# Kernel optimization log

Hardware: AMD Instinct MI355X
Metric: run time of the kernel (lower is better)

## Reference

```python
import jax, jax.numpy as jnp
import numpy as np

HIDDEN_DIM = 1024
HEAD_DIM = 64


def setup_inputs() -> dict:
    key = jax.random.key(0)
    kx, kq, kk, kv, ko = jax.random.split(key, 5)
    B, S = 4, 4096
    x = jax.random.normal(kx, (B, S, HIDDEN_DIM), dtype=jnp.float32)
    # nn.Linear(in, out, bias=False) weight has shape [out, in]; y = x @ W.T
    scale = 1.0 / np.sqrt(HIDDEN_DIM)
    Wq = jax.random.normal(kq, (HEAD_DIM, HIDDEN_DIM), dtype=jnp.float32) * scale
    Wk = jax.random.normal(kk, (HEAD_DIM, HIDDEN_DIM), dtype=jnp.float32) * scale
    Wv = jax.random.normal(kv, (HEAD_DIM, HIDDEN_DIM), dtype=jnp.float32) * scale
    Wo = jax.random.normal(ko, (HIDDEN_DIM, HEAD_DIM), dtype=jnp.float32) * (1.0 / np.sqrt(HEAD_DIM))
    return {"x": x, "Wq": Wq, "Wk": Wk, "Wv": Wv, "Wo": Wo}


def reference(x, Wq, Wk, Wv, Wo):
    # projections: x [B,S,H] @ W.T [H,D] -> [B,S,D]
    q = jnp.einsum('bsh,dh->bsd', x, Wq)
    k = jnp.einsum('bsh,dh->bsd', x, Wk)
    v = jnp.einsum('bsh,dh->bsd', x, Wv)
    d = q.shape[-1]
    scores = jnp.einsum('bqd,bkd->bqk', q, k) / jnp.sqrt(jnp.asarray(d, q.dtype))
    S = q.shape[1]
    causal_mask = jnp.triu(jnp.ones((S, S), dtype=bool), k=1)  # True above diagonal
    scores = jnp.where(causal_mask[None, :, :], jnp.asarray(-jnp.inf, scores.dtype), scores)
    attn = jax.nn.softmax(scores, axis=-1)
    out = jnp.einsum('bqk,bkd->bqd', attn, v)
    return jnp.einsum('bsd,hd->bsh', out, Wo)
```

## Files before the change

### kernel.cpp

```cpp
#include <hip/hip_runtime.h>
#include <hip/hip_bf16.h>


typedef __attribute__((ext_vector_type(8))) __bf16 bf16x8;
typedef __attribute__((ext_vector_type(4))) float f32x4;

#define BATCH 4
#define SEQ   4096
#define HID   1024
#define HDIM  64
#define CHT   8
#define NCMAX 8

__device__ __forceinline__ unsigned short f2bf(float f) {
  unsigned u = __builtin_bit_cast(unsigned, f);
  u += 0x7fffu + ((u >> 16) & 1u);
  return (unsigned short)(u >> 16);
}
__device__ __forceinline__ float bf2f(unsigned short u) {
  unsigned v = ((unsigned)u) << 16;
  return __builtin_bit_cast(float, v);
}
__device__ __forceinline__ __bf16 f2bf16(float f) {
  unsigned short us = f2bf(f);
  return __builtin_bit_cast(__bf16, us);
}
__device__ __forceinline__ bf16x8 pack8(f32x4 a, f32x4 b) {
  bf16x8 r;
  r[0] = f2bf16(a[0]); r[1] = f2bf16(a[1]); r[2] = f2bf16(a[2]); r[3] = f2bf16(a[3]);
  r[4] = f2bf16(b[0]); r[5] = f2bf16(b[1]); r[6] = f2bf16(b[2]); r[7] = f2bf16(b[3]);
  return r;
}

__global__ __launch_bounds__(256) void convert_w(
    const float* __restrict__ Wq, const float* __restrict__ Wk,
    const float* __restrict__ Wv, const float* __restrict__ Wo,
    unsigned short* __restrict__ q, unsigned short* __restrict__ k,
    unsigned short* __restrict__ v, unsigned short* __restrict__ o) {
  const int gid = blockIdx.x * 256 + threadIdx.x;
  const int mat = gid >> 16, idx = gid & 0xFFFF;
  const float* s = (mat == 0) ? Wq : (mat == 1) ? Wk : (mat == 2) ? Wv : Wo;
  unsigned short* d = (mat == 0) ? q : (mat == 1) ? k : (mat == 2) ? v : o;
  d[idx] = f2bf(s[idx]);
}

__global__ __launch_bounds__(256) void qkv_proj(
    const float* __restrict__ x,
    const unsigned short* __restrict__ Wqb,
    const unsigned short* __restrict__ Wkb,
    const unsigned short* __restrict__ Wvb,
    unsigned short* __restrict__ Q,
    unsigned short* __restrict__ K,
    unsigned short* __restrict__ Vt) {
  const int mb   = blockIdx.x;
  const int tid  = threadIdx.x;
  const int lane = tid & 63;
  const int wave = tid >> 6;
  const int quad = lane >> 4;
  const int l15  = lane & 15;
  const int rt   = wave >> 1;
  const int nh   = wave & 1;
  const int ar   = rt * 16 + l15;
  const int row0 = mb * 32 + rt * 16;

  __shared__ float xs[2][32 * 32];

  const unsigned short* Ws[3] = {Wqb, Wkb, Wvb};

  f32x4 acc[3][2];
  const f32x4 zero = {0.f, 0.f, 0.f, 0.f};
#pragma unroll
  for (int z = 0; z < 3; ++z)
#pragma unroll
    for (int n2 = 0; n2 < 2; ++n2) acc[z][n2] = zero;

  const int srow   = tid >> 3;
  const int schunk = (tid & 7) ^ (srow & 7);
  const float* sgp = x + (size_t)(mb * 32 + srow) * HID + schunk * 4;
  float* lb0 = &xs[0][wave * 256];
  float* lb1 = &xs[1][wave * 256];

  const int ra0 = ar * 32 + ((2 * quad)     ^ (ar & 7)) * 4;
  const int ra1 = ar * 32 + ((2 * quad + 1) ^ (ar & 7)) * 4;

  __builtin_amdgcn_global_load_lds(
      (const __attribute__((address_space(1))) void*)sgp,
      (__attribute__((address_space(3))) void*)lb0, 16, 0, 0);

  for (int kk = 0; kk < HID; kk += 32) {
    const int buf = (kk >> 5) & 1;
    __syncthreads();
    if (kk + 32 < HID) {
      __builtin_amdgcn_global_load_lds(
          (const __attribute__((address_space(1))) void*)(sgp + kk + 32),
          (__attribute__((address_space(3))) void*)(buf ? lb0 : lb1), 16, 0, 0);
    }
    f32x4 alo = *reinterpret_cast<const f32x4*>(&xs[buf][ra0]);
    f32x4 ahi = *reinterpret_cast<const f32x4*>(&xs[buf][ra1]);
    bf16x8 a = pack8(alo, ahi);
#pragma unroll
    for (int z = 0; z < 3; ++z)
#pragma unroll
      for (int n2 = 0; n2 < 2; ++n2) {
        const int col = nh * 32 + n2 * 16 + l15;
        bf16x8 b = *reinterpret_cast<const bf16x8*>(Ws[z] + (size_t)col * HID + kk + quad * 8);
        acc[z][n2] = __builtin_amdgcn_mfma_f32_16x16x32_bf16(a, b, acc[z][n2], 0, 0, 0);
      }
  }

#pragma unroll
  for (int z = 0; z < 2; ++z) {
    unsigned short* Out = (z == 0) ? Q : K;
#pragma unroll
    for (int n2 = 0; n2 < 2; ++n2)
#pragma unroll
      for (int r = 0; r < 4; ++r) {
        const int row = row0 + quad * 4 + r;
        const int col = nh * 32 + n2 * 16 + l15;
        Out[(size_t)row * HDIM + col] = f2bf(acc[z][n2][r]);
      }
  }
#pragma unroll
  for (int n2 = 0; n2 < 2; ++n2)
#pragma unroll
    for (int r = 0; r < 4; ++r) {
      const int row = row0 + quad * 4 + r;
      const int col = nh * 32 + n2 * 16 + l15;
      const int bb = row >> 12, sl = row & 4095;
      Vt[(size_t)bb * HDIM * SEQ + (size_t)col * SEQ + sl] = f2bf(acc[2][n2][r]);
    }
}

#define LSTR 72

__global__ __launch_bounds__(256) void flash_splitk(
    const unsigned short* __restrict__ Qg,
    const unsigned short* __restrict__ Kg,
    const unsigned short* __restrict__ Vt,
    unsigned short* __restrict__ Og,
    unsigned short* __restrict__ Opart,
    float2* __restrict__ Ml) {
  const int qb = blockIdx.x;
  const int b  = blockIdx.y;
  const int c  = blockIdx.z;
  const int nc = (qb >> 3) + 1;
  if (c >= nc) return;
  const int j0 = c * CHT;
  const int j1 = min(j0 + CHT, qb + 1);

  const int tid  = threadIdx.x;
  const int lane = tid & 63;
  const int wave = tid >> 6;
  const int quad = lane >> 4;
  const int l15  = lane & 15;

  __shared__ unsigned short kt[64 * LSTR];
  __shared__ unsigned short vt[64 * LSTR];
  __shared__ unsigned short pt[4][16 * LSTR];

  const size_t base  = (size_t)b * SEQ * HDIM;
  const size_t baseT = (size_t)b * HDIM * SEQ;
  const int qrow0 = qb * 64 + wave * 16;

  bf16x8 aq[2];
  {
    const unsigned short* qp = Qg + base + (size_t)(qrow0 + l15) * HDIM + quad * 8;
    aq[0] = *reinterpret_cast<const bf16x8*>(qp);
    aq[1] = *reinterpret_cast<const bf16x8*>(qp + 32);
  }

  f32x4 o[4];
  const f32x4 zero = {0.f, 0.f, 0.f, 0.f};
#pragma unroll
  for (int n = 0; n < 4; ++n) o[n] = zero;
  float m_i[4], l_i[4];
#pragma unroll
  for (int r = 0; r < 4; ++r) { m_i[r] = -__builtin_inff(); l_i[r] = 0.f; }

  unsigned short* pw = pt[wave];
  const int srow = tid >> 2, sc0 = (tid & 3) * 16;
  const unsigned short* kb = Kg + base;
  const unsigned short* vb = Vt + baseT;

  const float C = 0.125f * 1.44269504f;

  uint4 pk0, pk1, pv0, pv1;
  {
    const uint4* kp = reinterpret_cast<const uint4*>(kb + (size_t)(j0 * 64 + srow) * HDIM + sc0);
    pk0 = kp[0]; pk1 = kp[1];
    const uint4* vp = reinterpret_cast<const uint4*>(vb + (size_t)srow * SEQ + j0 * 64 + sc0);
    pv0 = vp[0]; pv1 = vp[1];
    *reinterpret_cast<uint4*>(&kt[srow * LSTR + sc0])     = pk0;
    *reinterpret_cast<uint4*>(&kt[srow * LSTR + sc0 + 8]) = pk1;
    *reinterpret_cast<uint4*>(&vt[srow * LSTR + sc0])     = pv0;
    *reinterpret_cast<uint4*>(&vt[srow * LSTR + sc0 + 8]) = pv1;
  }

  for (int j = j0; j < j1; ++j) {
    __syncthreads();
    const bool pre = (j + 1 < j1);
    if (pre) {
      const uint4* kp = reinterpret_cast<const uint4*>(kb + (size_t)((j + 1) * 64 + srow) * HDIM + sc0);
      pk0 = kp[0]; pk1 = kp[1];
      const uint4* vp = reinterpret_cast<const uint4*>(vb + (size_t)srow * SEQ + (j + 1) * 64 + sc0);
      pv0 = vp[0]; pv1 = vp[1];
    }

    f32x4 s[4];
#pragma unroll
    for (int n = 0; n < 4; ++n) s[n] = zero;
#pragma unroll
    for (int ks = 0; ks < 2; ++ks) {
#pragma unroll
      for (int n = 0; n < 4; ++n) {
        bf16x8 bk = *reinterpret_cast<const bf16x8*>(&kt[(n * 16 + l15) * LSTR + ks * 32 + quad * 8]);
        s[n] = __builtin_amdgcn_mfma_f32_16x16x32_bf16(aq[ks], bk, s[n], 0, 0, 0);
      }
    }

    if (j == qb) {
#pragma unroll
      for (int n = 0; n < 4; ++n) {
        const int col = n * 16 + l15;
#pragma unroll
        for (int r = 0; r < 4; ++r) {
          const int rowl = wave * 16 + quad * 4 + r;
          if (col > rowl) s[n][r] = -__builtin_inff();
        }
      }
    }

    float mnew[4], alpha[4], mC[4];
#pragma unroll
    for (int r = 0; r < 4; ++r) {
      float v = fmaxf(fmaxf(s[0][r], s[1][r]), fmaxf(s[2][r], s[3][r]));
#pragma unroll
      for (int off = 1; off < 16; off <<= 1) v = fmaxf(v, __shfl_xor(v, off, 64));
      mnew[r]  = fmaxf(m_i[r], v);
      alpha[r] = __builtin_amdgcn_exp2f((m_i[r] - mnew[r]) * C);
      mC[r]    = mnew[r] * C;
    }
    float p[4][4];
#pragma unroll
    for (int n = 0; n < 4; ++n)
#pragma unroll
      for (int r = 0; r < 4; ++r)
        p[n][r] = __builtin_amdgcn_exp2f(__builtin_fmaf(s[n][r], C, -mC[r]));
#pragma unroll
    for (int r = 0; r < 4; ++r) {
      float v = (p[0][r] + p[1][r]) + (p[2][r] + p[3][r]);
#pragma unroll
      for (int off = 1; off < 16; off <<= 1) v += __shfl_xor(v, off, 64);
      l_i[r] = l_i[r] * alpha[r] + v;
      m_i[r] = mnew[r];
    }
#pragma unroll
    for (int n = 0; n < 4; ++n)
#pragma unroll
      for (int r = 0; r < 4; ++r) o[n][r] *= alpha[r];

#pragma unroll
    for (int n = 0; n < 4; ++n)
#pragma unroll
      for (int r = 0; r < 4; ++r)
        pw[(quad * 4 + r) * LSTR + n * 16 + l15] = f2bf(p[n][r]);

#pragma unroll
    for (int ks = 0; ks < 2; ++ks) {
      bf16x8 ap = *reinterpret_cast<const bf16x8*>(&pw[l15 * LSTR + ks * 32 + quad * 8]);
#pragma unroll
      for (int n = 0; n < 4; ++n) {
        bf16x8 bv = *reinterpret_cast<const bf16x8*>(&vt[(n * 16 + l15) * LSTR + ks * 32 + quad * 8]);
        o[n] = __builtin_amdgcn_mfma_f32_16x16x32_bf16(ap, bv, o[n], 0, 0, 0);
      }
    }

    __syncthreads();
    if (pre) {
      *reinterpret_cast<uint4*>(&kt[srow * LSTR + sc0])     = pk0;
      *reinterpret_cast<uint4*>(&kt[srow * LSTR + sc0 + 8]) = pk1;
      *reinterpret_cast<uint4*>(&vt[srow * LSTR + sc0])     = pv0;
      *reinterpret_cast<uint4*>(&vt[srow * LSTR + sc0 + 8]) = pv1;
    }
  }

  if (nc == 1) {
#pragma unroll
    for (int n = 0; n < 4; ++n)
#pragma unroll
      for (int r = 0; r < 4; ++r) {
        const int row = qrow0 + quad * 4 + r;
        const int col = n * 16 + l15;
        Og[base + (size_t)row * HDIM + col] = f2bf(o[n][r] / l_i[r]);
      }
  } else {
    const int slot = ((b * 64 + qb) << 3) + c;
#pragma unroll
    for (int n = 0; n < 4; ++n)
#pragma unroll
      for (int r = 0; r < 4; ++r) {
        const int rowl = wave * 16 + quad * 4 + r;
        const int col  = n * 16 + l15;
        Opart[(size_t)slot * 4096 + rowl * 64 + col] = f2bf(o[n][r]);
      }
    if (l15 == 0) {
#pragma unroll
      for (int r = 0; r < 4; ++r) {
        const int rowl = wave * 16 + quad * 4 + r;
        Ml[slot * 64 + rowl] = make_float2(m_i[r], l_i[r]);
      }
    }
  }
}

__global__ __launch_bounds__(256) void merge_splitk(
    const unsigned short* __restrict__ Opart,
    const float2* __restrict__ Ml,
    unsigned short* __restrict__ Og) {
  const int qb = blockIdx.x;
  if (qb < CHT) return;
  const int b  = blockIdx.y;
  const int nc = (qb >> 3) + 1;
  const int row = threadIdx.x >> 2;
  const int cg  = (threadIdx.x & 3) * 16;
  const int slot0 = (b * 64 + qb) << 3;

  float m[NCMAX], l[NCMAX];
  float M = -__builtin_inff();
  for (int c = 0; c < nc; ++c) {
    float2 ml = Ml[(slot0 + c) * 64 + row];
    m[c] = ml.x; l[c] = ml.y;
    M = fmaxf(M, m[c]);
  }
  const float C = 0.125f * 1.44269504f;
  float L = 0.f, acc[16];
#pragma unroll
  for (int i = 0; i < 16; ++i) acc[i] = 0.f;
  for (int c = 0; c < nc; ++c) {
    const float w = __builtin_amdgcn_exp2f((m[c] - M) * C);
    L += w * l[c];
    const unsigned short* p = Opart + (size_t)(slot0 + c) * 4096 + row * 64 + cg;
    uint4 u0 = *reinterpret_cast<const uint4*>(p);
    uint4 u1 = *reinterpret_cast<const uint4*>(p + 8);
    const unsigned* uu = &u0.x;
#pragma unroll
    for (int i = 0; i < 4; ++i) {
      acc[2 * i]     += w * bf2f((unsigned short)(uu[i] & 0xFFFF));
      acc[2 * i + 1] += w * bf2f((unsigned short)(uu[i] >> 16));
    }
    const unsigned* vv = &u1.x;
#pragma unroll
    for (int i = 0; i < 4; ++i) {
      acc[8 + 2 * i]     += w * bf2f((unsigned short)(vv[i] & 0xFFFF));
      acc[8 + 2 * i + 1] += w * bf2f((unsigned short)(vv[i] >> 16));
    }
  }
  const float inv = 1.f / L;
  uint4 o0, o1;
  unsigned* po = &o0.x;
#pragma unroll
  for (int i = 0; i < 4; ++i)
    po[i] = (unsigned)f2bf(acc[2 * i] * inv) | ((unsigned)f2bf(acc[2 * i + 1] * inv) << 16);
  unsigned* p1 = &o1.x;
#pragma unroll
  for (int i = 0; i < 4; ++i)
    p1[i] = (unsigned)f2bf(acc[8 + 2 * i] * inv) | ((unsigned)f2bf(acc[8 + 2 * i + 1] * inv) << 16);
  unsigned short* dst = Og + (size_t)b * SEQ * HDIM + (size_t)(qb * 64 + row) * HDIM + cg;
  *reinterpret_cast<uint4*>(dst)     = o0;
  *reinterpret_cast<uint4*>(dst + 8) = o1;
}

__global__ __launch_bounds__(256) void out_proj(
    const unsigned short* __restrict__ O,
    const unsigned short* __restrict__ Wob,
    float* __restrict__ Y) {
  const int nb   = blockIdx.x;
  const int mb   = blockIdx.y;
  const int lane = threadIdx.x & 63;
  const int wave = threadIdx.x >> 6;
  const int quad = lane >> 4;
  const int l15  = lane & 15;
  const int row0 = mb * 64 + wave * 16;

  f32x4 acc[4];
  const f32x4 zero = {0.f, 0.f, 0.f, 0.f};
#pragma unroll
  for (int n = 0; n < 4; ++n) acc[n] = zero;

  const unsigned short* op = O + (size_t)(row0 + l15) * HDIM + quad * 8;
  bf16x8 a0 = *reinterpret_cast<const bf16x8*>(op);
  bf16x8 a1 = *reinterpret_cast<const bf16x8*>(op + 32);
#pragma unroll
  for (int n = 0; n < 4; ++n) {
    const int col = nb * 64 + n * 16 + l15;
    const unsigned short* wp = Wob + (size_t)col * HDIM + quad * 8;
    bf16x8 b0 = *reinterpret_cast<const bf16x8*>(wp);
    bf16x8 b1 = *reinterpret_cast<const bf16x8*>(wp + 32);
    acc[n] = __builtin_amdgcn_mfma_f32_16x16x32_bf16(a0, b0, acc[n], 0, 0, 0);
    acc[n] = __builtin_amdgcn_mfma_f32_16x16x32_bf16(a1, b1, acc[n], 0, 0, 0);
  }
#pragma unroll
  for (int n = 0; n < 4; ++n)
#pragma unroll
    for (int r = 0; r < 4; ++r) {
      const int row = row0 + quad * 4 + r;
      const int col = nb * 64 + n * 16 + l15;
      Y[(size_t)row * HID + col] = acc[n][r];
    }
}

extern "C" void kernel_launch(void* const* d_in, const int* in_sizes, int n_in,
                              void* d_out, int out_size, void* d_ws, size_t ws_size,
                              hipStream_t stream) {
  const float* x  = (const float*)d_in[0];
  const float* Wq = (const float*)d_in[1];
  const float* Wk = (const float*)d_in[2];
  const float* Wv = (const float*)d_in[3];
  const float* Wo = (const float*)d_in[4];
  float* Y = (float*)d_out;

  const size_t qkv_elems = (size_t)BATCH * SEQ * HDIM;
  const size_t w_elems   = (size_t)HDIM * HID;
  unsigned short* Q     = (unsigned short*)d_ws;
  unsigned short* K     = Q + qkv_elems;
  unsigned short* Vt    = K + qkv_elems;
  unsigned short* O     = Vt + qkv_elems;
  unsigned short* Wqb   = O + qkv_elems;
  unsigned short* Wkb   = Wqb + w_elems;
  unsigned short* Wvb   = Wkb + w_elems;
  unsigned short* Wob   = Wvb + w_elems;
  unsigned short* Opart = (unsigned short*)d_out;
  float2*         Ml    = (float2*)(Opart + (size_t)2048 * 4096);

  convert_w   <<<1024,               256, 0, stream>>>(Wq, Wk, Wv, Wo, Wqb, Wkb, Wvb, Wob);
  qkv_proj    <<<512,                256, 0, stream>>>(x, Wqb, Wkb, Wvb, Q, K, Vt);
  flash_splitk<<<dim3(64, 4, NCMAX), 256, 0, stream>>>(Q, K, Vt, O, Opart, Ml);
  merge_splitk<<<dim3(64, 4),        256, 0, stream>>>(Opart, Ml, O);
  out_proj    <<<dim3(16, 256),      256, 0, stream>>>(O, Wob, Y);
}
```

Before: 239.2 us.

## Shrink QKV projection tile to 16 rows, load x directly without LDS

Rewrites the QKV projection kernel so each block handles 16 rows instead of 32. Each wave now computes one 16-column slice of Q, K and V, reading x straight from global memory instead of staging it through double-buffered LDS with async global-to-LDS loads. This removes the per-iteration barrier and the LDS traffic, and doubles the grid to improve occupancy. The cost is that all four waves redundantly load the same x rows from global or cache, each with strided 32-byte accesses per lane, and there is no software prefetch overlap.

```diff
diff --git a/kernel.cpp b/kernel.cpp
--- a/kernel.cpp
+++ b/kernel.cpp
@@ -58,77 +58,43 @@
   const int wave = tid >> 6;
   const int quad = lane >> 4;
   const int l15  = lane & 15;
-  const int rt   = wave >> 1;
-  const int nh   = wave & 1;
-  const int ar   = rt * 16 + l15;
-  const int row0 = mb * 32 + rt * 16;
-
-  __shared__ float xs[2][32 * 32];
-
-  const unsigned short* Ws[3] = {Wqb, Wkb, Wvb};
-
-  f32x4 acc[3][2];
+
+  const int arow = mb * 16 + l15;
+  const float* xp = x + (size_t)arow * HID + quad * 8;
+
+  const int col = wave * 16 + l15;
+  const unsigned short* bq = Wqb + (size_t)col * HID + quad * 8;
+  const unsigned short* bk = Wkb + (size_t)col * HID + quad * 8;
+  const unsigned short* bv = Wvb + (size_t)col * HID + quad * 8;
+
   const f32x4 zero = {0.f, 0.f, 0.f, 0.f};
-#pragma unroll
-  for (int z = 0; z < 3; ++z)
-#pragma unroll
-    for (int n2 = 0; n2 < 2; ++n2) acc[z][n2] = zero;
-
-  const int srow   = tid >> 3;
-  const int schunk = (tid & 7) ^ (srow & 7);
-  const float* sgp = x + (size_t)(mb * 32 + srow) * HID + schunk * 4;
-  float* lb0 = &xs[0][wave * 256];
-  float* lb1 = &xs[1][wave * 256];
-
-  const int ra0 = ar * 32 + ((2 * quad)     ^ (ar & 7)) * 4;
-  const int ra1 = ar * 32 + ((2 * quad + 1) ^ (ar & 7)) * 4;
-
-  __builtin_amdgcn_global_load_lds(
-      (const __attribute__((address_space(1))) void*)sgp,
-      (__attribute__((address_space(3))) void*)lb0, 16, 0, 0);
-
+  f32x4 accq = zero, acck = zero, accv = zero;
+
+#pragma unroll 2
   for (int kk = 0; kk < HID; kk += 32) {
-    const int buf = (kk >> 5) & 1;
-    __syncthreads();
-    if (kk + 32 < HID) {
-      __builtin_amdgcn_global_load_lds(
-          (const __attribute__((address_space(1))) void*)(sgp + kk + 32),
-          (__attribute__((address_space(3))) void*)(buf ? lb0 : lb1), 16, 0, 0);
-    }
-    f32x4 alo = *reinterpret_cast<const f32x4*>(&xs[buf][ra0]);
-    f32x4 ahi = *reinterpret_cast<const f32x4*>(&xs[buf][ra1]);
-    bf16x8 a = pack8(alo, ahi);
-#pragma unroll
-    for (int z = 0; z < 3; ++z)
-#pragma unroll
-      for (int n2 = 0; n2 < 2; ++n2) {
-        const int col = nh * 32 + n2 * 16 + l15;
-        bf16x8 b = *reinterpret_cast<const bf16x8*>(Ws[z] + (size_t)col * HID + kk + quad * 8);
-        acc[z][n2] = __builtin_amdgcn_mfma_f32_16x16x32_bf16(a, b, acc[z][n2], 0, 0, 0);
-      }
-  }
-
-#pragma unroll
-  for (int z = 0; z < 2; ++z) {
-    unsigned short* Out = (z == 0) ? Q : K;
-#pragma unroll
-    for (int n2 = 0; n2 < 2; ++n2)
-#pragma unroll
-      for (int r = 0; r < 4; ++r) {
-        const int row = row0 + quad * 4 + r;
-        const int col = nh * 32 + n2 * 16 + l15;
-        Out[(size_t)row * HDIM + col] = f2bf(acc[z][n2][r]);
-      }
-  }
-#pragma unroll
-  for (int n2 = 0; n2 < 2; ++n2)
-#pragma unroll
-    for (int r = 0; r < 4; ++r) {
-      const int row = row0 + quad * 4 + r;
-      const int col = nh * 32 + n2 * 16 + l15;
-      const int bb = row >> 12, sl = row & 4095;
-      Vt[(size_t)bb * HDIM * SEQ + (size_t)col * SEQ + sl] = f2bf(acc[2][n2][r]);
-    }
+    f32x4 alo = *reinterpret_cast<const f32x4*>(xp + kk);
+    f32x4 ahi = *reinterpret_cast<const f32x4*>(xp + kk + 4);
+    bf16x8 b0 = *reinterpret_cast<const bf16x8*>(bq + kk);
+    bf16x8 b1 = *reinterpret_cast<const bf16x8*>(bk + kk);
+    bf16x8 b2 = *reinterpret_cast<const bf16x8*>(bv + kk);
+    bf16x8 a  = pack8(alo, ahi);
+    accq = __builtin_amdgcn_mfma_f32_16x16x32_bf16(a, b0, accq, 0, 0, 0);
+    acck = __builtin_amdgcn_mfma_f32_16x16x32_bf16(a, b1, acck, 0, 0, 0);
+    accv = __builtin_amdgcn_mfma_f32_16x16x32_bf16(a, b2, accv, 0, 0, 0);
+  }
+
+  const int row0 = mb * 16 + quad * 4;
+#pragma unroll
+  for (int r = 0; r < 4; ++r) {
+    Q[(size_t)(row0 + r) * HDIM + col] = f2bf(accq[r]);
+    K[(size_t)(row0 + r) * HDIM + col] = f2bf(acck[r]);
+  }
+#pragma unroll
+  for (int r = 0; r < 4; ++r) {
+    const int row = row0 + r;
+    const int bb = row >> 12, sl = row & 4095;
+    Vt[(size_t)bb * HDIM * SEQ + (size_t)col * SEQ + sl] = f2bf(accv[r]);
+  }
 }
 
 #define LSTR 72
@@ -433,7 +399,7 @@
   float2*         Ml    = (float2*)(Opart + (size_t)2048 * 4096);
 
   convert_w   <<<1024,               256, 0, stream>>>(Wq, Wk, Wv, Wo, Wqb, Wkb, Wvb, Wob);
-  qkv_proj    <<<512,                256, 0, stream>>>(x, Wqb, Wkb, Wvb, Q, K, Vt);
+  qkv_proj    <<<1024,               256, 0, stream>>>(x, Wqb, Wkb, Wvb, Q, K, Vt);
   flash_splitk<<<dim3(64, 4, NCMAX), 256, 0, stream>>>(Q, K, Vt, O, Opart, Ml);
   merge_splitk<<<dim3(64, 4),        256, 0, stream>>>(Opart, Ml, O);
   out_proj    <<<dim3(16, 256),      256, 0, stream>>>(O, Wob, Y);
```

New measurement: 251.5 us. 1.05x slower.

## Stage QKV weights through LDS and widen projection K-tile to 64

Applied to the files above, without the earlier changes.

The QKV projection kernel now loads Wq/Wk/Wv tiles into double-buffered, swizzled LDS with async global_load_lds, instead of having every wave read them straight from global memory. The K step doubles from 32 to 64, so there are half as many barriers per tile. This targets redundant global/L2 weight traffic and load latency in the projection. It costs about 48KB of extra LDS per block, which may reduce occupancy, and the projection is only part of the total time.

```diff
diff --git a/kernel.cpp b/kernel.cpp
--- a/kernel.cpp
+++ b/kernel.cpp
@@ -63,7 +63,8 @@
   const int ar   = rt * 16 + l15;
   const int row0 = mb * 32 + rt * 16;
 
-  __shared__ float xs[2][32 * 32];
+  __shared__ float          xs[2][32 * 64];
+  __shared__ unsigned short wl[2][3 * 64 * 64];
 
   const unsigned short* Ws[3] = {Wqb, Wkb, Wvb};
 
@@ -74,39 +75,70 @@
 #pragma unroll
     for (int n2 = 0; n2 < 2; ++n2) acc[z][n2] = zero;
 
-  const int srow   = tid >> 3;
-  const int schunk = (tid & 7) ^ (srow & 7);
-  const float* sgp = x + (size_t)(mb * 32 + srow) * HID + schunk * 4;
-  float* lb0 = &xs[0][wave * 256];
-  float* lb1 = &xs[1][wave * 256];
-
-  const int ra0 = ar * 32 + ((2 * quad)     ^ (ar & 7)) * 4;
-  const int ra1 = ar * 32 + ((2 * quad + 1) ^ (ar & 7)) * 4;
-
-  __builtin_amdgcn_global_load_lds(
-      (const __attribute__((address_space(1))) void*)sgp,
-      (__attribute__((address_space(3))) void*)lb0, 16, 0, 0);
-
-  for (int kk = 0; kk < HID; kk += 32) {
-    const int buf = (kk >> 5) & 1;
+  const int xrow0 = tid >> 4;
+  const int xp    = tid & 15;
+  const int xg0   = (xp & 8) | ((xp & 7) ^ (xrow0 & 7));
+  const int xrow1 = xrow0 + 16;
+  const int xg1   = (xp & 8) | ((xp & 7) ^ (xrow1 & 7));
+  const float* xsrc0 = x + (size_t)(mb * 32 + xrow0) * HID + xg0 * 4;
+  const float* xsrc1 = x + (size_t)(mb * 32 + xrow1) * HID + xg1 * 4;
+  const int wcol0 = tid >> 3;
+  const int wp    = tid & 7;
+  const int wg0   = wp ^ (wcol0 & 7);
+  const int wcol1 = wcol0 + 32;
+  const int wg1   = wp ^ (wcol1 & 7);
+
+  const int swz = ar & 7;
+
+#define STAGE_TILE(buf, kk)                                                     \
+  do {                                                                          \
+    float* xb = &xs[buf][wave * 256];                                           \
+    __builtin_amdgcn_global_load_lds(                                           \
+        (const __attribute__((address_space(1))) void*)(xsrc0 + (kk)),          \
+        (__attribute__((address_space(3))) void*)xb, 16, 0, 0);                 \
+    __builtin_amdgcn_global_load_lds(                                           \
+        (const __attribute__((address_space(1))) void*)(xsrc1 + (kk)),          \
+        (__attribute__((address_space(3))) void*)(xb + 1024), 16, 0, 0);        \
+    _Pragma("unroll")                                                           \
+    for (int z = 0; z < 3; ++z) {                                               \
+      unsigned short* wb = &wl[buf][z * 4096 + wave * 512];                     \
+      __builtin_amdgcn_global_load_lds(                                         \
+          (const __attribute__((address_space(1))) void*)(                      \
+              Ws[z] + (size_t)wcol0 * HID + (kk) + wg0 * 8),                    \
+          (__attribute__((address_space(3))) void*)wb, 16, 0, 0);               \
+      __builtin_amdgcn_global_load_lds(                                         \
+          (const __attribute__((address_space(1))) void*)(                      \
+              Ws[z] + (size_t)wcol1 * HID + (kk) + wg1 * 8),                    \
+          (__attribute__((address_space(3))) void*)(wb + 2048), 16, 0, 0);      \
+    }                                                                           \
+  } while (0)
+
+  STAGE_TILE(0, 0);
+
+  for (int kk = 0; kk < HID; kk += 64) {
+    const int buf = (kk >> 6) & 1;
     __syncthreads();
-    if (kk + 32 < HID) {
-      __builtin_amdgcn_global_load_lds(
-          (const __attribute__((address_space(1))) void*)(sgp + kk + 32),
-          (__attribute__((address_space(3))) void*)(buf ? lb0 : lb1), 16, 0, 0);
-    }
-    f32x4 alo = *reinterpret_cast<const f32x4*>(&xs[buf][ra0]);
-    f32x4 ahi = *reinterpret_cast<const f32x4*>(&xs[buf][ra1]);
-    bf16x8 a = pack8(alo, ahi);
-#pragma unroll
-    for (int z = 0; z < 3; ++z)
-#pragma unroll
-      for (int n2 = 0; n2 < 2; ++n2) {
-        const int col = nh * 32 + n2 * 16 + l15;
-        bf16x8 b = *reinterpret_cast<const bf16x8*>(Ws[z] + (size_t)col * HID + kk + quad * 8);
-        acc[z][n2] = __builtin_amdgcn_mfma_f32_16x16x32_bf16(a, b, acc[z][n2], 0, 0, 0);
-      }
-  }
+    if (kk + 64 < HID) STAGE_TILE(buf ^ 1, kk + 64);
+
+#pragma unroll
+    for (int sub = 0; sub < 2; ++sub) {
+      const int c0 = sub * 8 + ((2 * quad)     ^ swz);
+      const int c1 = sub * 8 + ((2 * quad + 1) ^ swz);
+      f32x4 alo = *reinterpret_cast<const f32x4*>(&xs[buf][ar * 64 + c0 * 4]);
+      f32x4 ahi = *reinterpret_cast<const f32x4*>(&xs[buf][ar * 64 + c1 * 4]);
+      bf16x8 a = pack8(alo, ahi);
+#pragma unroll
+      for (int z = 0; z < 3; ++z)
+#pragma unroll
+        for (int n2 = 0; n2 < 2; ++n2) {
+          const int col = nh * 32 + n2 * 16 + l15;
+          const int wc  = (sub * 4 + quad) ^ (col & 7);
+          bf16x8 b = *reinterpret_cast<const bf16x8*>(&wl[buf][z * 4096 + col * 64 + wc * 8]);
+          acc[z][n2] = __builtin_amdgcn_mfma_f32_16x16x32_bf16(a, b, acc[z][n2], 0, 0, 0);
+        }
+    }
+  }
+#undef STAGE_TILE
 
 #pragma unroll
   for (int z = 0; z < 2; ++z) {
```

Measured after the change: 203.0 us. -15.1%, faster.
